# Performance work log

Measured on AMD Instinct MI355X. Metric: run time of the kernel, lower is better.

Reference implementation:

```python
import jax, jax.numpy as jnp
import numpy as np

N, E, B = 50000, 400000, 128
F_IN, EDIM, EMB, H = 64, 8, 64, 4
HC = EMB * H  # 256
L = 3          # gnn_layers
DN = 256       # dense_neurons
NEG_SLOPE = 0.2
EPS = 1e-5


def setup_inputs():
    key = jax.random.key(0)
    ks = jax.random.split(key, 32)
    s = 0.05
    d = {}
    d["x"] = jax.random.normal(ks[0], (N, F_IN), jnp.float32)
    d["edge_index"] = jax.random.randint(ks[1], (2, E), 0, N, jnp.int32)
    d["edge_attr"] = jax.random.normal(ks[2], (E, EDIM), jnp.float32)
    d["mol_formal_charge"] = jax.random.normal(ks[3], (B,), jnp.float32)
    d["mol_nrot"] = jax.random.normal(ks[4], (B,), jnp.float32)
    d["batch_index"] = jnp.sort(jax.random.randint(ks[5], (N,), 0, B, jnp.int32))
    # GATv2 params, stacked over L layers (in_dim == EMB == F_IN for all layers)
    d["gat_Wl"] = jax.random.normal(ks[6], (L, F_IN, HC), jnp.float32) * s
    d["gat_Wr"] = jax.random.normal(ks[7], (L, F_IN, HC), jnp.float32) * s
    d["gat_We"] = jax.random.normal(ks[8], (L, EDIM, HC), jnp.float32) * s
    d["gat_att"] = jax.random.normal(ks[9], (L, H, EMB), jnp.float32) * s
    d["gat_b"] = jnp.zeros((L, HC), jnp.float32)
    d["tr_W"] = jax.random.normal(ks[10], (L, HC, EMB), jnp.float32) * s
    d["tr_b"] = jnp.zeros((L, EMB), jnp.float32)
    d["bn_g"] = jnp.ones((L, EMB), jnp.float32)
    d["bn_b"] = jnp.zeros((L, EMB), jnp.float32)
    d["gate_W"] = jax.random.normal(ks[11], (EMB, 1), jnp.float32) * s
    d["gate_b"] = jnp.zeros((1,), jnp.float32)
    d["lin1_W"] = jax.random.normal(ks[12], (EMB + 2, DN), jnp.float32) * s
    d["lin1_b"] = jnp.zeros((DN,), jnp.float32)
    d["fc1_W"] = jax.random.normal(ks[13], (DN, DN // 2), jnp.float32) * s
    d["fc1_b"] = jnp.zeros((DN // 2,), jnp.float32)
    d["fc2_W"] = jax.random.normal(ks[14], (DN // 2, DN // 4), jnp.float32) * s
    d["fc2_b"] = jnp.zeros((DN // 4,), jnp.float32)
    d["out_W"] = jax.random.normal(ks[15], (DN // 4, 1), jnp.float32) * s
    d["out_b"] = jnp.zeros((1,), jnp.float32)
    return d


def _seg_softmax(logits, seg, num):
    # numerically stable per-segment softmax over leading axis
    mx = jax.ops.segment_max(logits, seg, num_segments=num)
    ex = jnp.exp(logits - mx[seg])
    den = jax.ops.segment_sum(ex, seg, num_segments=num)
    return ex / den[seg]


def reference(x, edge_index, edge_attr, mol_formal_charge, mol_nrot, batch_index,
              gat_Wl, gat_Wr, gat_We, gat_att, gat_b, tr_W, tr_b, bn_g, bn_b,
              gate_W, gate_b, lin1_W, lin1_b, fc1_W, fc1_b, fc2_W, fc2_b,
              out_W, out_b):
    src, dst = edge_index[0], edge_index[1]  # messages flow src -> dst
    h = x
    for l in range(L):
        xl = (h @ gat_Wl[l]).reshape(N, H, EMB)
        xr = (h @ gat_Wr[l]).reshape(N, H, EMB)
        ea = (edge_attr @ gat_We[l]).reshape(E, H, EMB)
        xls = xl[src]                                   # [E,H,C]
        m = jax.nn.leaky_relu(xls + xr[dst] + ea, NEG_SLOPE)
        logit = jnp.einsum('ehc,hc->eh', m, gat_att[l])  # [E,H]
        alpha = _seg_softmax(logit, dst, N)              # [E,H]
        agg = jax.ops.segment_sum(alpha[:, :, None] * xls, dst, num_segments=N)
        h = agg.reshape(N, HC) + gat_b[l]
        h = jax.nn.relu(h @ tr_W[l] + tr_b[l])
        # BatchNorm1d (training-mode batch stats, biased var)
        mu = h.mean(0)
        var = h.var(0)
        h = (h - mu) / jnp.sqrt(var + EPS) * bn_g[l] + bn_b[l]
    # AttentionalAggregation pooling
    gate = h @ gate_W + gate_b                           # [N,1]
    w = _seg_softmax(gate, batch_index, B)
    pooled = jax.ops.segment_sum(w * h, batch_index, num_segments=B)  # [B,EMB]
    z = jnp.concatenate([pooled, mol_formal_charge[:, None], mol_nrot[:, None]], axis=1)
    z = jax.nn.relu(z @ lin1_W + lin1_b)
    z = jax.nn.relu(z @ fc1_W + fc1_b)
    z = jax.nn.relu(z @ fc2_W + fc2_b)
    return z @ out_W + out_b                             # [B,1]
```

## Files before the change

### kernel.cpp

```cpp
#include <hip/hip_runtime.h>

#define NN 50000
#define NE 400000
#define NB 128
#define NINF (-__builtin_inff())

__device__ __forceinline__ float dpp_add16(float x) {
    int v = __float_as_int(x);
    x += __int_as_float(__builtin_amdgcn_update_dpp(0, v, 0xB1, 0xF, 0xF, true));
    v = __float_as_int(x);
    x += __int_as_float(__builtin_amdgcn_update_dpp(0, v, 0x4E, 0xF, 0xF, true));
    v = __float_as_int(x);
    x += __int_as_float(__builtin_amdgcn_update_dpp(0, v, 0x141, 0xF, 0xF, true));
    v = __float_as_int(x);
    x += __int_as_float(__builtin_amdgcn_update_dpp(0, v, 0x140, 0xF, 0xF, true));
    return x;
}

__global__ __launch_bounds__(256) void k_hist(const int* __restrict__ dstv, int* __restrict__ deg) {
    int e = blockIdx.x * 256 + threadIdx.x;
    if (e < NE) atomicAdd(&deg[dstv[e]], 1);
}

__global__ __launch_bounds__(256) void k_scan1(const int* __restrict__ deg, int* __restrict__ bsum) {
    __shared__ int ws[4];
    const int tid = threadIdx.x, lane = tid & 63, w = tid >> 6;
    const int i = blockIdx.x * 256 + tid;
    int v = (i < NN) ? deg[i] : 0;
    #pragma unroll
    for (int off = 32; off; off >>= 1) v += __shfl_xor(v, off);
    if (lane == 0) ws[w] = v;
    __syncthreads();
    if (tid == 0) bsum[blockIdx.x] = ws[0] + ws[1] + ws[2] + ws[3];
}

__global__ __launch_bounds__(256) void k_scan2(const int* __restrict__ bsum, int* __restrict__ boff, int nblk) {
    __shared__ int ws[4];
    const int tid = threadIdx.x, lane = tid & 63, w = tid >> 6;
    int v = (tid < nblk) ? bsum[tid] : 0;
    int incl = v;
    #pragma unroll
    for (int off = 1; off < 64; off <<= 1) {
        int t = __shfl_up(incl, off);
        if (lane >= off) incl += t;
    }
    if (lane == 63) ws[w] = incl;
    __syncthreads();
    int add = 0;
    for (int k = 0; k < w; ++k) add += ws[k];
    if (tid < nblk) boff[tid] = add + incl - v;
}

__global__ __launch_bounds__(256) void k_scan3(const int* __restrict__ deg, const int* __restrict__ boff,
                                               int* __restrict__ rowptr) {
    __shared__ int ws[4];
    const int tid = threadIdx.x, lane = tid & 63, w = tid >> 6;
    const int i = blockIdx.x * 256 + tid;
    int v = (i < NN) ? deg[i] : 0;
    int incl = v;
    #pragma unroll
    for (int off = 1; off < 64; off <<= 1) {
        int t = __shfl_up(incl, off);
        if (lane >= off) incl += t;
    }
    if (lane == 63) ws[w] = incl;
    __syncthreads();
    int add = boff[blockIdx.x];
    for (int k = 0; k < w; ++k) add += ws[k];
    if (i < NN) rowptr[i + 1] = add + incl;
    if (i == 0) rowptr[0] = 0;
}

__global__ __launch_bounds__(256) void k_scatter(const int* __restrict__ dstv, const int* __restrict__ srcv,
                                                 const float* __restrict__ eattr, const int* __restrict__ rowptr,
                                                 int* __restrict__ cnt, int* __restrict__ eid,
                                                 int* __restrict__ src_perm, float4* __restrict__ ea_perm,
                                                 int use_perm) {
    int e = blockIdx.x * 256 + threadIdx.x;
    if (e < NE) {
        int d = dstv[e];
        int pos = rowptr[d] + atomicAdd(&cnt[d], 1);
        eid[pos] = e;
        if (use_perm) {
            src_perm[pos] = srcv[e];
            ea_perm[(size_t)pos * 2] = ((const float4*)eattr)[e * 2];
            ea_perm[(size_t)pos * 2 + 1] = ((const float4*)eattr)[e * 2 + 1];
        }
    }
}

__global__ __launch_bounds__(256, 4) void k_gemm64(const float* __restrict__ A, const float* __restrict__ Wl,
                                                   const float* __restrict__ Wr, float* __restrict__ Cl,
                                                   float* __restrict__ Cr, const float* __restrict__ stats,
                                                   const float* __restrict__ bg, const float* __restrict__ bb) {
    __shared__ float At[32 * 132];
    __shared__ float Ws[32 * 128];
    __shared__ float sc_s[64], sh_s[64], shW_s[128];
    const int tid = threadIdx.x;
    const int mat = blockIdx.y >> 1, ch = blockIdx.y & 1;
    const float* W = mat ? Wr : Wl;
    float* C = mat ? Cr : Cl;
    const int r0b = blockIdx.x * 128;
    const int cg = tid & 15;
    const int rg = tid >> 4;

    if (stats) {
        if (tid < 64) {
            const float mu = stats[tid] * (1.0f / (float)NN);
            const float var = stats[64 + tid] * (1.0f / (float)NN) - mu * mu;
            const float rstd = rsqrtf(var + 1e-5f);
            const float sc = bg[tid] * rstd;
            sc_s[tid] = sc;
            sh_s[tid] = fmaf(-mu, sc, bb[tid]);
        }
        __syncthreads();
        if (tid < 128) {
            const float* wc = W + ch * 128 + tid;
            float s = 0.f;
            for (int k = 0; k < 64; ++k) s = fmaf(sh_s[k], wc[k * 256], s);
            shW_s[tid] = s;
        }
        __syncthreads();
    }

    float acc[8][8];
    if (stats) {
        #pragma unroll
        for (int rr = 0; rr < 8; ++rr)
            #pragma unroll
            for (int j = 0; j < 8; ++j)
                acc[rr][j] = (j < 4) ? shW_s[cg * 4 + j] : shW_s[64 + cg * 4 + (j - 4)];
    } else {
        #pragma unroll
        for (int rr = 0; rr < 8; ++rr)
            #pragma unroll
            for (int j = 0; j < 8; ++j) acc[rr][j] = 0.f;
    }

    for (int kc = 0; kc < 2; ++kc) {
        if (kc) __syncthreads();
        for (int i = tid; i < 1024; i += 256) {
            const int k = i >> 5, c4 = i & 31;
            float4 v = ((const float4*)W)[(kc * 32 + k) * 64 + ch * 32 + c4];
            if (stats) {
                const float s = sc_s[kc * 32 + k];
                v.x *= s; v.y *= s; v.z *= s; v.w *= s;
            }
            ((float4*)Ws)[i] = v;
        }
        for (int i = tid; i < 1024; i += 256) {
            const int r = i >> 3, c4 = i & 7;
            const int rgl = (r0b + r < NN) ? (r0b + r) : (NN - 1);
            const float4 v = ((const float4*)A)[rgl * 16 + kc * 8 + c4];
            At[(c4 * 4 + 0) * 132 + r] = v.x;
            At[(c4 * 4 + 1) * 132 + r] = v.y;
            At[(c4 * 4 + 2) * 132 + r] = v.z;
            At[(c4 * 4 + 3) * 132 + r] = v.w;
        }
        __syncthreads();
        #pragma unroll 4
        for (int k = 0; k < 32; ++k) {
            const float4 a0 = *(const float4*)(At + k * 132 + rg * 8);
            const float4 a1 = *(const float4*)(At + k * 132 + rg * 8 + 4);
            const float4 w0 = *(const float4*)(Ws + k * 128 + cg * 4);
            const float4 w1 = *(const float4*)(Ws + k * 128 + 64 + cg * 4);
            const float ar[8] = {a0.x, a0.y, a0.z, a0.w, a1.x, a1.y, a1.z, a1.w};
            #pragma unroll
            for (int rr = 0; rr < 8; ++rr) {
                acc[rr][0] = fmaf(ar[rr], w0.x, acc[rr][0]);
                acc[rr][1] = fmaf(ar[rr], w0.y, acc[rr][1]);
                acc[rr][2] = fmaf(ar[rr], w0.z, acc[rr][2]);
                acc[rr][3] = fmaf(ar[rr], w0.w, acc[rr][3]);
                acc[rr][4] = fmaf(ar[rr], w1.x, acc[rr][4]);
                acc[rr][5] = fmaf(ar[rr], w1.y, acc[rr][5]);
                acc[rr][6] = fmaf(ar[rr], w1.z, acc[rr][6]);
                acc[rr][7] = fmaf(ar[rr], w1.w, acc[rr][7]);
            }
        }
    }
    #pragma unroll
    for (int rr = 0; rr < 8; ++rr) {
        const int r = r0b + rg * 8 + rr;
        if (r < NN) {
            float* cp = C + (size_t)r * 256 + ch * 128 + cg * 4;
            *(float4*)cp = make_float4(acc[rr][0], acc[rr][1], acc[rr][2], acc[rr][3]);
            *(float4*)(cp + 64) = make_float4(acc[rr][4], acc[rr][5], acc[rr][6], acc[rr][7]);
        }
    }
}

template <bool PERM>
__global__ __launch_bounds__(256, 4) void k_agg(const float* __restrict__ xl, float* __restrict__ xragg,
                                                const float* __restrict__ att, const float* __restrict__ gatb,
                                                const int* __restrict__ rowptr, const int* __restrict__ eid,
                                                const int* __restrict__ srcv, const float* __restrict__ eattr,
                                                const int* __restrict__ src_perm, const float4* __restrict__ ea_perm,
                                                const float* __restrict__ We) {
    const int lane = threadIdx.x & 63;
    const float4 we0 = ((const float4*)(We + 0 * 256))[lane];
    const float4 we1 = ((const float4*)(We + 1 * 256))[lane];
    const float4 we2 = ((const float4*)(We + 2 * 256))[lane];
    const float4 we3 = ((const float4*)(We + 3 * 256))[lane];
    const float4 we4 = ((const float4*)(We + 4 * 256))[lane];
    const float4 we5 = ((const float4*)(We + 5 * 256))[lane];
    const float4 we6 = ((const float4*)(We + 6 * 256))[lane];
    const float4 we7 = ((const float4*)(We + 7 * 256))[lane];
    const float4 attf = ((const float4*)att)[lane];
    const float4 gbf = ((const float4*)gatb)[lane];
    const int nw = gridDim.x * (blockDim.x >> 6);
    int wid = blockIdx.x * (blockDim.x >> 6) + (threadIdx.x >> 6);

#define LOADE(X, idx)                                                          \
    {                                                                          \
        int s_;                                                                \
        const float4* eap_;                                                    \
        if (PERM) {                                                            \
            s_ = src_perm[idx];                                                \
            eap_ = ea_perm + (size_t)(idx) * 2;                                \
        } else {                                                               \
            const int e_ = eid[idx];                                           \
            s_ = srcv[e_];                                                     \
            eap_ = (const float4*)(eattr + (size_t)e_ * 8);                    \
        }                                                                      \
        X##x = ((const float4*)(xl + (size_t)s_ * 256))[lane];                 \
        X##a = eap_[0];                                                        \
        X##b = eap_[1];                                                        \
    }

#define PROC(X)                                                                \
    {                                                                          \
        float v0 = fmaf(X##a.x, we0.x, xr.x), v1 = fmaf(X##a.x, we0.y, xr.y);  \
        float v2 = fmaf(X##a.x, we0.z, xr.z), v3 = fmaf(X##a.x, we0.w, xr.w);  \
        v0 = fmaf(X##a.y, we1.x, v0); v1 = fmaf(X##a.y, we1.y, v1);            \
        v2 = fmaf(X##a.y, we1.z, v2); v3 = fmaf(X##a.y, we1.w, v3);            \
        v0 = fmaf(X##a.z, we2.x, v0); v1 = fmaf(X##a.z, we2.y, v1);            \
        v2 = fmaf(X##a.z, we2.z, v2); v3 = fmaf(X##a.z, we2.w, v3);            \
        v0 = fmaf(X##a.w, we3.x, v0); v1 = fmaf(X##a.w, we3.y, v1);            \
        v2 = fmaf(X##a.w, we3.z, v2); v3 = fmaf(X##a.w, we3.w, v3);            \
        v0 = fmaf(X##b.x, we4.x, v0); v1 = fmaf(X##b.x, we4.y, v1);            \
        v2 = fmaf(X##b.x, we4.z, v2); v3 = fmaf(X##b.x, we4.w, v3);            \
        v0 = fmaf(X##b.y, we5.x, v0); v1 = fmaf(X##b.y, we5.y, v1);            \
        v2 = fmaf(X##b.y, we5.z, v2); v3 = fmaf(X##b.y, we5.w, v3);            \
        v0 = fmaf(X##b.z, we6.x, v0); v1 = fmaf(X##b.z, we6.y, v1);            \
        v2 = fmaf(X##b.z, we6.z, v2); v3 = fmaf(X##b.z, we6.w, v3);            \
        v0 = fmaf(X##b.w, we7.x, v0); v1 = fmaf(X##b.w, we7.y, v1);            \
        v2 = fmaf(X##b.w, we7.z, v2); v3 = fmaf(X##b.w, we7.w, v3);            \
        v0 += X##x.x; v1 += X##x.y; v2 += X##x.z; v3 += X##x.w;                \
        v0 = fmaxf(v0, 0.2f * v0); v1 = fmaxf(v1, 0.2f * v1);                  \
        v2 = fmaxf(v2, 0.2f * v2); v3 = fmaxf(v3, 0.2f * v3);                  \
        float part = v0 * attf.x;                                              \
        part = fmaf(v1, attf.y, part);                                         \
        part = fmaf(v2, attf.z, part);                                         \
        part = fmaf(v3, attf.w, part);                                         \
        part = dpp_add16(part);                                                \
        const float p = __expf(part);                                          \
        den += p;                                                              \
        c0 = fmaf(p, X##x.x, c0);                                              \
        c1 = fmaf(p, X##x.y, c1);                                              \
        c2 = fmaf(p, X##x.z, c2);                                              \
        c3 = fmaf(p, X##x.w, c3);                                              \
    }

    for (int n = wid; n < NN; n += nw) {
        const int e0 = rowptr[n], e1 = rowptr[n + 1];
        const float4 xr = ((const float4*)(xragg + (size_t)n * 256))[lane];
        float den = 0.f, c0 = 0.f, c1 = 0.f, c2 = 0.f, c3 = 0.f;
        float4 Ax, Aa, Ab, Bx, Ba, Bb, Cx, Ca, Cb;
        const int cnt = e1 - e0;
        if (cnt > 0) {
            LOADE(A, e0);
            if (cnt > 1) LOADE(B, e0 + 1);
            if (cnt > 2) LOADE(C, e0 + 2);
            int i = e0;
            for (; i + 5 < e1; i += 3) {
                PROC(A);
                LOADE(A, i + 3);
                PROC(B);
                LOADE(B, i + 4);
                PROC(C);
                LOADE(C, i + 5);
            }
            const int m = e1 - i;
            PROC(A);
            if (m >= 2) PROC(B);
            if (m >= 3) PROC(C);
            if (m >= 4) { LOADE(A, i + 3); PROC(A); }
            if (m == 5) { LOADE(B, i + 4); PROC(B); }
        }
        float4 o;
        if (cnt > 0) {
            const float inv = 1.0f / den;
            o.x = fmaf(c0, inv, gbf.x);
            o.y = fmaf(c1, inv, gbf.y);
            o.z = fmaf(c2, inv, gbf.z);
            o.w = fmaf(c3, inv, gbf.w);
        } else {
            o = gbf;
        }
        ((float4*)(xragg + (size_t)n * 256))[lane] = o;
    }
#undef LOADE
#undef PROC
}

__global__ __launch_bounds__(256, 4) void k_tr(const float* __restrict__ A, const float* __restrict__ W,
                                               const float* __restrict__ bias, float* __restrict__ Hout,
                                               float* __restrict__ stats) {
    __shared__ float At[32 * 260];
    __shared__ float Ws[32 * 64];
    __shared__ float red[128];
    const int tid = threadIdx.x;
    const int cg = tid & 7;
    const int rg = tid >> 3;
    const int r0b = blockIdx.x * 256;

    float acc[8][8];
    #pragma unroll
    for (int rr = 0; rr < 8; ++rr)
        #pragma unroll
        for (int j = 0; j < 8; ++j)
            acc[rr][j] = bias[cg * 8 + j];

    for (int kc = 0; kc < 8; ++kc) {
        if (kc) __syncthreads();
        for (int i = tid; i < 512; i += 256)
            ((float4*)Ws)[i] = ((const float4*)(W + kc * 2048))[i];
        for (int i = tid; i < 2048; i += 256) {
            const int r = i >> 3, c4 = i & 7;
            const int rgl = (r0b + r < NN) ? (r0b + r) : (NN - 1);
            const float4 v = ((const float4*)A)[(size_t)rgl * 64 + kc * 8 + c4];
            At[(c4 * 4 + 0) * 260 + r] = v.x;
            At[(c4 * 4 + 1) * 260 + r] = v.y;
            At[(c4 * 4 + 2) * 260 + r] = v.z;
            At[(c4 * 4 + 3) * 260 + r] = v.w;
        }
        __syncthreads();
        #pragma unroll 4
        for (int k = 0; k < 32; ++k) {
            const float4 a0 = *(const float4*)(At + k * 260 + rg * 8);
            const float4 a1 = *(const float4*)(At + k * 260 + rg * 8 + 4);
            const float4 w0 = *(const float4*)(Ws + k * 64 + cg * 8);
            const float4 w1 = *(const float4*)(Ws + k * 64 + cg * 8 + 4);
            const float ar[8] = {a0.x, a0.y, a0.z, a0.w, a1.x, a1.y, a1.z, a1.w};
            #pragma unroll
            for (int rr = 0; rr < 8; ++rr) {
                acc[rr][0] = fmaf(ar[rr], w0.x, acc[rr][0]);
                acc[rr][1] = fmaf(ar[rr], w0.y, acc[rr][1]);
                acc[rr][2] = fmaf(ar[rr], w0.z, acc[rr][2]);
                acc[rr][3] = fmaf(ar[rr], w0.w, acc[rr][3]);
                acc[rr][4] = fmaf(ar[rr], w1.x, acc[rr][4]);
                acc[rr][5] = fmaf(ar[rr], w1.y, acc[rr][5]);
                acc[rr][6] = fmaf(ar[rr], w1.z, acc[rr][6]);
                acc[rr][7] = fmaf(ar[rr], w1.w, acc[rr][7]);
            }
        }
    }
    float lsum[8], lsq[8];
    #pragma unroll
    for (int j = 0; j < 8; ++j) { lsum[j] = 0.f; lsq[j] = 0.f; }
    #pragma unroll
    for (int rr = 0; rr < 8; ++rr) {
        const int r = r0b + rg * 8 + rr;
        if (r < NN) {
            float v[8];
            #pragma unroll
            for (int j = 0; j < 8; ++j) {
                v[j] = fmaxf(acc[rr][j], 0.f);
                lsum[j] += v[j];
                lsq[j] = fmaf(v[j], v[j], lsq[j]);
            }
            float* hp = Hout + (size_t)r * 64;
            *(float4*)(hp + cg * 8) = make_float4(v[0], v[1], v[2], v[3]);
            *(float4*)(hp + cg * 8 + 4) = make_float4(v[4], v[5], v[6], v[7]);
        }
    }
    __syncthreads();
    if (tid < 128) red[tid] = 0.f;
    __syncthreads();
    #pragma unroll
    for (int j = 0; j < 8; ++j) {
        atomicAdd(&red[cg * 8 + j], lsum[j]);
        atomicAdd(&red[64 + cg * 8 + j], lsq[j]);
    }
    __syncthreads();
    if (tid < 64) {
        atomicAdd(&stats[tid], red[tid]);
        atomicAdd(&stats[64 + tid], red[64 + tid]);
    }
}

__global__ __launch_bounds__(256) void k_poolhead(const float* __restrict__ h, const float* __restrict__ gw,
                                                  const int* __restrict__ bidx, const float* __restrict__ stats,
                                                  const float* __restrict__ bg, const float* __restrict__ bb,
                                                  const float* __restrict__ fc, const float* __restrict__ nrot,
                                                  const float* __restrict__ W1, const float* __restrict__ b1,
                                                  const float* __restrict__ W2, const float* __restrict__ b2,
                                                  const float* __restrict__ W3, const float* __restrict__ b3,
                                                  const float* __restrict__ W4, const float* __restrict__ b4,
                                                  float* __restrict__ out) {
    __shared__ float gate_s[1024];
    __shared__ float red[4];
    __shared__ float pp[4][64];
    __shared__ float scb[64], shb[64];
    __shared__ float z[66], a1[256], a2[128], a3[64];
    const int b = blockIdx.x, tid = threadIdx.x, lane = tid & 63, w = tid >> 6;
    if (tid < 64) {
        const float mu = stats[tid] * (1.0f / (float)NN);
        const float var = stats[64 + tid] * (1.0f / (float)NN) - mu * mu;
        const float rstd = rsqrtf(var + 1e-5f);
        const float sc = bg[tid] * rstd;
        scb[tid] = sc;
        shb[tid] = fmaf(-mu, sc, bb[tid]);
    }
    int lo = 0, hi = NN;
    while (lo < hi) { int mid = (lo + hi) >> 1; if (bidx[mid] < b) lo = mid + 1; else hi = mid; }
    const int s0 = lo;
    lo = 0; hi = NN;
    while (lo < hi) { int mid = (lo + hi) >> 1; if (bidx[mid] < b + 1) lo = mid + 1; else hi = mid; }
    const int s1 = lo;
    const int seg = s1 - s0;
    __syncthreads();

    const float gwv = gw[lane] * scb[lane];
    for (int i = s0 + w; i < s1; i += 4) {
        float p = h[(size_t)i * 64 + lane] * gwv;
        #pragma unroll
        for (int off = 32; off; off >>= 1) p += __shfl_xor(p, off);
        if (lane == 0) gate_s[i - s0] = p;
    }
    __syncthreads();
    float v = NINF;
    for (int i = tid; i < seg; i += 256) v = fmaxf(v, gate_s[i]);
    #pragma unroll
    for (int off = 32; off; off >>= 1) v = fmaxf(v, __shfl_xor(v, off));
    if (lane == 0) red[w] = v;
    __syncthreads();
    const float mx = fmaxf(fmaxf(red[0], red[1]), fmaxf(red[2], red[3]));
    __syncthreads();
    float d = 0.f;
    for (int i = tid; i < seg; i += 256) {
        const float ex = __expf(gate_s[i] - mx);
        gate_s[i] = ex;
        d += ex;
    }
    #pragma unroll
    for (int off = 32; off; off >>= 1) d += __shfl_xor(d, off);
    if (lane == 0) red[w] = d;
    __syncthreads();
    const float den = red[0] + red[1] + red[2] + red[3];
    const int c = tid & 63, ro = tid >> 6;
    float acc = 0.f;
    for (int i = s0 + ro; i < s1; i += 4) acc = fmaf(gate_s[i - s0], h[(size_t)i * 64 + c], acc);
    pp[ro][c] = acc;
    __syncthreads();
    if (tid < 64) {
        const float raw = (pp[0][tid] + pp[1][tid] + pp[2][tid] + pp[3][tid]) / den;
        z[tid] = (seg > 0) ? fmaf(raw, scb[tid], shb[tid]) : shb[tid];
    }
    if (tid == 64) z[64] = fc[b];
    if (tid == 65) z[65] = nrot[b];
    __syncthreads();
    float s = b1[tid];
    for (int k = 0; k < 66; ++k) s = fmaf(z[k], W1[k * 256 + tid], s);
    a1[tid] = fmaxf(s, 0.f);
    __syncthreads();
    if (tid < 128) {
        float s2 = b2[tid];
        for (int k = 0; k < 256; ++k) s2 = fmaf(a1[k], W2[k * 128 + tid], s2);
        a2[tid] = fmaxf(s2, 0.f);
    }
    __syncthreads();
    if (tid < 64) {
        float s3 = b3[tid];
        for (int k = 0; k < 128; ++k) s3 = fmaf(a2[k], W3[k * 64 + tid], s3);
        a3[tid] = fmaxf(s3, 0.f);
    }
    __syncthreads();
    if (tid < 64) {
        float p = a3[tid] * W4[tid];
        #pragma unroll
        for (int off = 32; off; off >>= 1) p += __shfl_xor(p, off);
        if (tid == 0) out[b] = p + b4[0];
    }
}

extern "C" void kernel_launch(void* const* d_in, const int* in_sizes, int n_in,
                              void* d_out, int out_size, void* d_ws, size_t ws_size,
                              hipStream_t stream) {
    const float* x     = (const float*)d_in[0];
    const int*   ei    = (const int*)d_in[1];
    const float* eattr = (const float*)d_in[2];
    const float* fcv   = (const float*)d_in[3];
    const float* nrot  = (const float*)d_in[4];
    const int*   bidx  = (const int*)d_in[5];
    const float* Wl    = (const float*)d_in[6];
    const float* Wr    = (const float*)d_in[7];
    const float* We    = (const float*)d_in[8];
    const float* att   = (const float*)d_in[9];
    const float* gatb  = (const float*)d_in[10];
    const float* trW   = (const float*)d_in[11];
    const float* trb   = (const float*)d_in[12];
    const float* bng   = (const float*)d_in[13];
    const float* bnb   = (const float*)d_in[14];
    const float* gateW = (const float*)d_in[15];
    const float* W1    = (const float*)d_in[17];
    const float* b1    = (const float*)d_in[18];
    const float* W2    = (const float*)d_in[19];
    const float* b2    = (const float*)d_in[20];
    const float* W3    = (const float*)d_in[21];
    const float* b3    = (const float*)d_in[22];
    const float* W4    = (const float*)d_in[23];
    const float* b4    = (const float*)d_in[24];
    float* out = (float*)d_out;

    const int* srcv = ei;
    const int* dstv = ei + NE;

    char* w = (char*)d_ws;
    float*  xl       = (float*)(w);
    float*  xragg    = (float*)(w + 51200000);
    float*  hbuf     = (float*)(w + 102400000);
    int*    deg      = (int*)  (w + 102400000);
    int*    cnt      = (int*)  (w + 102600000);
    int*    eid      = (int*)  (w + 115200000);
    int*    rowptr   = (int*)  (w + 116800000);
    float*  stats    = (float*)(w + 117000064);
    int*    bsum     = (int*)  (w + 117004096);
    int*    boff     = (int*)  (w + 117006144);
    int*    src_perm = (int*)  (w + 117042048);
    float4* ea_perm  = (float4*)(w + 118642048);
    const bool use_perm = (ws_size >= (size_t)131442048);
    const int NBLK = (NN + 255) / 256;

    hipMemsetAsync(deg, 0, 400000, stream);
    hipMemsetAsync(stats, 0, 1536, stream);
    k_hist<<<(NE + 255) / 256, 256, 0, stream>>>(dstv, deg);
    k_scan1<<<NBLK, 256, 0, stream>>>(deg, bsum);
    k_scan2<<<1, 256, 0, stream>>>(bsum, boff, NBLK);
    k_scan3<<<NBLK, 256, 0, stream>>>(deg, boff, rowptr);
    k_scatter<<<(NE + 255) / 256, 256, 0, stream>>>(dstv, srcv, eattr, rowptr, cnt, eid,
                                                    src_perm, ea_perm, use_perm ? 1 : 0);

    const float* hin = x;
    for (int l = 0; l < 3; ++l) {
        const float* st = (l == 0) ? nullptr : (stats + (l - 1) * 128);
        const float* g  = (l == 0) ? nullptr : (bng + (l - 1) * 64);
        const float* bb = (l == 0) ? nullptr : (bnb + (l - 1) * 64);
        dim3 gg((NN + 127) / 128, 4);
        k_gemm64<<<gg, 256, 0, stream>>>(hin, Wl + l * 16384, Wr + l * 16384, xl, xragg, st, g, bb);
        if (use_perm)
            k_agg<true><<<2048, 256, 0, stream>>>(xl, xragg, att + l * 256, gatb + l * 256, rowptr,
                                                  eid, srcv, eattr, src_perm, ea_perm, We + l * 2048);
        else
            k_agg<false><<<2048, 256, 0, stream>>>(xl, xragg, att + l * 256, gatb + l * 256, rowptr,
                                                   eid, srcv, eattr, src_perm, ea_perm, We + l * 2048);
        k_tr<<<(NN + 255) / 256, 256, 0, stream>>>(xragg, trW + l * 16384, trb + l * 64, hbuf, stats + l * 128);
        hin = hbuf;
    }
    k_poolhead<<<NB, 256, 0, stream>>>(hbuf, gateW, bidx, stats + 2 * 128, bng + 128, bnb + 128,
                                       fcv, nrot, W1, b1, W2, b2, W3, b3, W4, b4, out);
}
```

Before: 698.6 us.

## Prefetch next node's metadata in GAT aggregation and fold memsets into scan kernels

New measurement: 713.2 us. 2.1% more time.

```diff
diff --git a/kernel.cpp b/kernel.cpp
--- a/kernel.cpp
+++ b/kernel.cpp
@@ -22,10 +22,12 @@
     if (e < NE) atomicAdd(&deg[dstv[e]], 1);
 }
 
-__global__ __launch_bounds__(256) void k_scan1(const int* __restrict__ deg, int* __restrict__ bsum) {
+__global__ __launch_bounds__(256) void k_scan1(const int* __restrict__ deg, int* __restrict__ bsum,
+                                               int* __restrict__ cnt) {
     __shared__ int ws[4];
     const int tid = threadIdx.x, lane = tid & 63, w = tid >> 6;
     const int i = blockIdx.x * 256 + tid;
+    if (i < NN) cnt[i] = 0;
     int v = (i < NN) ? deg[i] : 0;
     #pragma unroll
     for (int off = 32; off; off >>= 1) v += __shfl_xor(v, off);
@@ -34,9 +36,11 @@
     if (tid == 0) bsum[blockIdx.x] = ws[0] + ws[1] + ws[2] + ws[3];
 }
 
-__global__ __launch_bounds__(256) void k_scan2(const int* __restrict__ bsum, int* __restrict__ boff, int nblk) {
+__global__ __launch_bounds__(256) void k_scan2(const int* __restrict__ bsum, int* __restrict__ boff, int nblk,
+                                               float* __restrict__ stats) {
     __shared__ int ws[4];
     const int tid = threadIdx.x, lane = tid & 63, w = tid >> 6;
+    for (int i = tid; i < 384; i += 256) stats[i] = 0.f;
     int v = (tid < nblk) ? bsum[tid] : 0;
     int incl = v;
     #pragma unroll
@@ -208,7 +212,7 @@
     const float4 attf = ((const float4*)att)[lane];
     const float4 gbf = ((const float4*)gatb)[lane];
     const int nw = gridDim.x * (blockDim.x >> 6);
-    int wid = blockIdx.x * (blockDim.x >> 6) + (threadIdx.x >> 6);
+    const int wid = blockIdx.x * (blockDim.x >> 6) + (threadIdx.x >> 6);
 
 #define LOADE(X, idx)                                                          \
     {                                                                          \
@@ -261,9 +265,19 @@
         c3 = fmaf(p, X##x.w, c3);                                              \
     }
 
-    for (int n = wid; n < NN; n += nw) {
-        const int e0 = rowptr[n], e1 = rowptr[n + 1];
-        const float4 xr = ((const float4*)(xragg + (size_t)n * 256))[lane];
+    int n = wid;
+    if (n >= NN) return;
+    float4 xr = ((const float4*)(xragg + (size_t)n * 256))[lane];
+    int e0 = rowptr[n], e1 = rowptr[n + 1];
+    while (true) {
+        const int n2 = n + nw;
+        float4 xr2;
+        int e02 = 0, e12 = 0;
+        if (n2 < NN) {
+            xr2 = ((const float4*)(xragg + (size_t)n2 * 256))[lane];
+            e02 = rowptr[n2];
+            e12 = rowptr[n2 + 1];
+        }
         float den = 0.f, c0 = 0.f, c1 = 0.f, c2 = 0.f, c3 = 0.f;
         float4 Ax, Aa, Ab, Bx, Ba, Bb, Cx, Ca, Cb;
         const int cnt = e1 - e0;
@@ -298,6 +312,8 @@
             o = gbf;
         }
         ((float4*)(xragg + (size_t)n * 256))[lane] = o;
+        if (n2 >= NN) break;
+        n = n2; xr = xr2; e0 = e02; e1 = e12;
     }
 #undef LOADE
 #undef PROC
@@ -532,11 +548,10 @@
     const bool use_perm = (ws_size >= (size_t)131442048);
     const int NBLK = (NN + 255) / 256;
 
-    hipMemsetAsync(deg, 0, 400000, stream);
-    hipMemsetAsync(stats, 0, 1536, stream);
+    hipMemsetAsync(deg, 0, 200000, stream);
     k_hist<<<(NE + 255) / 256, 256, 0, stream>>>(dstv, deg);
-    k_scan1<<<NBLK, 256, 0, stream>>>(deg, bsum);
-    k_scan2<<<1, 256, 0, stream>>>(bsum, boff, NBLK);
+    k_scan1<<<NBLK, 256, 0, stream>>>(deg, bsum, cnt);
+    k_scan2<<<1, 256, 0, stream>>>(bsum, boff, NBLK, stats);
     k_scan3<<<NBLK, 256, 0, stream>>>(deg, boff, rowptr);
     k_scatter<<<(NE + 255) / 256, 256, 0, stream>>>(dstv, srcv, eattr, rowptr, cnt, eid,
                                                     src_perm, ea_perm, use_perm ? 1 : 0);
@@ -549,10 +564,10 @@
         dim3 gg((NN + 127) / 128, 4);
         k_gemm64<<<gg, 256, 0, stream>>>(hin, Wl + l * 16384, Wr + l * 16384, xl, xragg, st, g, bb);
         if (use_perm)
-            k_agg<true><<<2048, 256, 0, stream>>>(xl, xragg, att + l * 256, gatb + l * 256, rowptr,
+            k_agg<true><<<4096, 256, 0, stream>>>(xl, xragg, att + l * 256, gatb + l * 256, rowptr,
                                                   eid, srcv, eattr, src_perm, ea_perm, We + l * 2048);
         else
-            k_agg<false><<<2048, 256, 0, stream>>>(xl, xragg, att + l * 256, gatb + l * 256, rowptr,
+            k_agg<false><<<4096, 256, 0, stream>>>(xl, xragg, att + l * 256, gatb + l * 256, rowptr,
                                                    eid, srcv, eattr, src_perm, ea_perm, We + l * 2048);
         k_tr<<<(NN + 255) / 256, 256, 0, stream>>>(xragg, trW + l * 16384, trb + l * 64, hbuf, stats + l * 128);
         hin = hbuf;
```

## Hoist BatchNorm fold into tiny kernel, shrink GEMM K-tiles, fold memsets into scans

Applied to the files above, without the earlier changes.

New measurement: 1.394 ms. +99.5%, slower.

```diff
diff --git a/kernel.cpp b/kernel.cpp
--- a/kernel.cpp
+++ b/kernel.cpp
@@ -22,10 +22,12 @@
     if (e < NE) atomicAdd(&deg[dstv[e]], 1);
 }
 
-__global__ __launch_bounds__(256) void k_scan1(const int* __restrict__ deg, int* __restrict__ bsum) {
+__global__ __launch_bounds__(256) void k_scan1(const int* __restrict__ deg, int* __restrict__ bsum,
+                                               int* __restrict__ cnt) {
     __shared__ int ws[4];
     const int tid = threadIdx.x, lane = tid & 63, w = tid >> 6;
     const int i = blockIdx.x * 256 + tid;
+    if (i < NN) cnt[i] = 0;
     int v = (i < NN) ? deg[i] : 0;
     #pragma unroll
     for (int off = 32; off; off >>= 1) v += __shfl_xor(v, off);
@@ -34,9 +36,11 @@
     if (tid == 0) bsum[blockIdx.x] = ws[0] + ws[1] + ws[2] + ws[3];
 }
 
-__global__ __launch_bounds__(256) void k_scan2(const int* __restrict__ bsum, int* __restrict__ boff, int nblk) {
+__global__ __launch_bounds__(256) void k_scan2(const int* __restrict__ bsum, int* __restrict__ boff, int nblk,
+                                               float* __restrict__ stats) {
     __shared__ int ws[4];
     const int tid = threadIdx.x, lane = tid & 63, w = tid >> 6;
+    for (int i = tid; i < 2304; i += 256) stats[i] = 0.f;
     int v = (tid < nblk) ? bsum[tid] : 0;
     int incl = v;
     #pragma unroll
@@ -89,13 +93,36 @@
     }
 }
 
-__global__ __launch_bounds__(256, 4) void k_gemm64(const float* __restrict__ A, const float* __restrict__ Wl,
+__global__ __launch_bounds__(256) void k_bnfin(float* __restrict__ st, const float* __restrict__ g,
+                                               const float* __restrict__ b, const float* __restrict__ Wln,
+                                               const float* __restrict__ Wrn) {
+    __shared__ float sh_s[64];
+    const int tid = threadIdx.x;
+    if (tid < 64) {
+        const float mu = st[tid] * (1.0f / (float)NN);
+        const float var = st[64 + tid] * (1.0f / (float)NN) - mu * mu;
+        const float rstd = rsqrtf(var + 1e-5f);
+        const float sc = g[tid] * rstd;
+        const float sh = fmaf(-mu, sc, b[tid]);
+        st[128 + tid] = sc;
+        st[192 + tid] = sh;
+        sh_s[tid] = sh;
+    }
+    __syncthreads();
+    float al = 0.f, ar = 0.f;
+    for (int k = 0; k < 64; ++k) {
+        al = fmaf(sh_s[k], Wln[k * 256 + tid], al);
+        ar = fmaf(sh_s[k], Wrn[k * 256 + tid], ar);
+    }
+    st[256 + tid] = al;
+    st[512 + tid] = ar;
+}
+
+__global__ __launch_bounds__(256, 5) void k_gemm64(const float* __restrict__ A, const float* __restrict__ Wl,
                                                    const float* __restrict__ Wr, float* __restrict__ Cl,
-                                                   float* __restrict__ Cr, const float* __restrict__ stats,
-                                                   const float* __restrict__ bg, const float* __restrict__ bb) {
-    __shared__ float At[32 * 132];
-    __shared__ float Ws[32 * 128];
-    __shared__ float sc_s[64], sh_s[64], shW_s[128];
+                                                   float* __restrict__ Cr, const float* __restrict__ stats) {
+    __shared__ float At[16 * 132];
+    __shared__ float Ws[16 * 128];
     const int tid = threadIdx.x;
     const int mat = blockIdx.y >> 1, ch = blockIdx.y & 1;
     const float* W = mat ? Wr : Wl;
@@ -104,32 +131,16 @@
     const int cg = tid & 15;
     const int rg = tid >> 4;
 
-    if (stats) {
-        if (tid < 64) {
-            const float mu = stats[tid] * (1.0f / (float)NN);
-            const float var = stats[64 + tid] * (1.0f / (float)NN) - mu * mu;
-            const float rstd = rsqrtf(var + 1e-5f);
-            const float sc = bg[tid] * rstd;
-            sc_s[tid] = sc;
-            sh_s[tid] = fmaf(-mu, sc, bb[tid]);
-        }
-        __syncthreads();
-        if (tid < 128) {
-            const float* wc = W + ch * 128 + tid;
-            float s = 0.f;
-            for (int k = 0; k < 64; ++k) s = fmaf(sh_s[k], wc[k * 256], s);
-            shW_s[tid] = s;
-        }
-        __syncthreads();
-    }
-
     float acc[8][8];
     if (stats) {
+        const float* shW = stats + 256 + mat * 256 + ch * 128;
+        const float4 i0 = *(const float4*)(shW + cg * 4);
+        const float4 i1 = *(const float4*)(shW + 64 + cg * 4);
         #pragma unroll
-        for (int rr = 0; rr < 8; ++rr)
-            #pragma unroll
-            for (int j = 0; j < 8; ++j)
-                acc[rr][j] = (j < 4) ? shW_s[cg * 4 + j] : shW_s[64 + cg * 4 + (j - 4)];
+        for (int rr = 0; rr < 8; ++rr) {
+            acc[rr][0] = i0.x; acc[rr][1] = i0.y; acc[rr][2] = i0.z; acc[rr][3] = i0.w;
+            acc[rr][4] = i1.x; acc[rr][5] = i1.y; acc[rr][6] = i1.z; acc[rr][7] = i1.w;
+        }
     } else {
         #pragma unroll
         for (int rr = 0; rr < 8; ++rr)
@@ -137,21 +148,21 @@
             for (int j = 0; j < 8; ++j) acc[rr][j] = 0.f;
     }
 
-    for (int kc = 0; kc < 2; ++kc) {
+    for (int kc = 0; kc < 4; ++kc) {
         if (kc) __syncthreads();
-        for (int i = tid; i < 1024; i += 256) {
+        for (int i = tid; i < 512; i += 256) {
             const int k = i >> 5, c4 = i & 31;
-            float4 v = ((const float4*)W)[(kc * 32 + k) * 64 + ch * 32 + c4];
+            float4 v = ((const float4*)W)[(kc * 16 + k) * 64 + ch * 32 + c4];
             if (stats) {
-                const float s = sc_s[kc * 32 + k];
+                const float s = stats[128 + kc * 16 + k];
                 v.x *= s; v.y *= s; v.z *= s; v.w *= s;
             }
             ((float4*)Ws)[i] = v;
         }
-        for (int i = tid; i < 1024; i += 256) {
-            const int r = i >> 3, c4 = i & 7;
+        for (int i = tid; i < 512; i += 256) {
+            const int r = i >> 2, c4 = i & 3;
             const int rgl = (r0b + r < NN) ? (r0b + r) : (NN - 1);
-            const float4 v = ((const float4*)A)[rgl * 16 + kc * 8 + c4];
+            const float4 v = ((const float4*)A)[rgl * 16 + kc * 4 + c4];
             At[(c4 * 4 + 0) * 132 + r] = v.x;
             At[(c4 * 4 + 1) * 132 + r] = v.y;
             At[(c4 * 4 + 2) * 132 + r] = v.z;
@@ -159,7 +170,7 @@
         }
         __syncthreads();
         #pragma unroll 4
-        for (int k = 0; k < 32; ++k) {
+        for (int k = 0; k < 16; ++k) {
             const float4 a0 = *(const float4*)(At + k * 132 + rg * 8);
             const float4 a1 = *(const float4*)(At + k * 132 + rg * 8 + 4);
             const float4 w0 = *(const float4*)(Ws + k * 128 + cg * 4);
@@ -208,7 +219,7 @@
     const float4 attf = ((const float4*)att)[lane];
     const float4 gbf = ((const float4*)gatb)[lane];
     const int nw = gridDim.x * (blockDim.x >> 6);
-    int wid = blockIdx.x * (blockDim.x >> 6) + (threadIdx.x >> 6);
+    const int wid = blockIdx.x * (blockDim.x >> 6) + (threadIdx.x >> 6);
 
 #define LOADE(X, idx)                                                          \
     {                                                                          \
@@ -303,11 +314,11 @@
 #undef PROC
 }
 
-__global__ __launch_bounds__(256, 4) void k_tr(const float* __restrict__ A, const float* __restrict__ W,
+__global__ __launch_bounds__(256, 5) void k_tr(const float* __restrict__ A, const float* __restrict__ W,
                                                const float* __restrict__ bias, float* __restrict__ Hout,
                                                float* __restrict__ stats) {
-    __shared__ float At[32 * 260];
-    __shared__ float Ws[32 * 64];
+    __shared__ float At[16 * 260];
+    __shared__ float Ws[16 * 64];
     __shared__ float red[128];
     const int tid = threadIdx.x;
     const int cg = tid & 7;
@@ -321,14 +332,13 @@
         for (int j = 0; j < 8; ++j)
             acc[rr][j] = bias[cg * 8 + j];
 
-    for (int kc = 0; kc < 8; ++kc) {
+    for (int kc = 0; kc < 16; ++kc) {
         if (kc) __syncthreads();
-        for (int i = tid; i < 512; i += 256)
-            ((float4*)Ws)[i] = ((const float4*)(W + kc * 2048))[i];
-        for (int i = tid; i < 2048; i += 256) {
-            const int r = i >> 3, c4 = i & 7;
+        if (tid < 256) ((float4*)Ws)[tid] = ((const float4*)(W + kc * 1024))[tid];
+        for (int i = tid; i < 1024; i += 256) {
+            const int r = i >> 2, c4 = i & 3;
             const int rgl = (r0b + r < NN) ? (r0b + r) : (NN - 1);
-            const float4 v = ((const float4*)A)[(size_t)rgl * 64 + kc * 8 + c4];
+            const float4 v = ((const float4*)A)[(size_t)rgl * 64 + kc * 4 + c4];
             At[(c4 * 4 + 0) * 260 + r] = v.x;
             At[(c4 * 4 + 1) * 260 + r] = v.y;
             At[(c4 * 4 + 2) * 260 + r] = v.z;
@@ -336,7 +346,7 @@
         }
         __syncthreads();
         #pragma unroll 4
-        for (int k = 0; k < 32; ++k) {
+        for (int k = 0; k < 16; ++k) {
             const float4 a0 = *(const float4*)(At + k * 260 + rg * 8);
             const float4 a1 = *(const float4*)(At + k * 260 + rg * 8 + 4);
             const float4 w0 = *(const float4*)(Ws + k * 64 + cg * 8);
@@ -525,38 +535,38 @@
     int*    eid      = (int*)  (w + 115200000);
     int*    rowptr   = (int*)  (w + 116800000);
     float*  stats    = (float*)(w + 117000064);
-    int*    bsum     = (int*)  (w + 117004096);
-    int*    boff     = (int*)  (w + 117006144);
+    int*    bsum     = (int*)  (w + 117010176);
+    int*    boff     = (int*)  (w + 117012224);
     int*    src_perm = (int*)  (w + 117042048);
     float4* ea_perm  = (float4*)(w + 118642048);
     const bool use_perm = (ws_size >= (size_t)131442048);
     const int NBLK = (NN + 255) / 256;
 
-    hipMemsetAsync(deg, 0, 400000, stream);
-    hipMemsetAsync(stats, 0, 1536, stream);
+    hipMemsetAsync(deg, 0, 200000, stream);
     k_hist<<<(NE + 255) / 256, 256, 0, stream>>>(dstv, deg);
-    k_scan1<<<NBLK, 256, 0, stream>>>(deg, bsum);
-    k_scan2<<<1, 256, 0, stream>>>(bsum, boff, NBLK);
+    k_scan1<<<NBLK, 256, 0, stream>>>(deg, bsum, cnt);
+    k_scan2<<<1, 256, 0, stream>>>(bsum, boff, NBLK, stats);
     k_scan3<<<NBLK, 256, 0, stream>>>(deg, boff, rowptr);
     k_scatter<<<(NE + 255) / 256, 256, 0, stream>>>(dstv, srcv, eattr, rowptr, cnt, eid,
                                                     src_perm, ea_perm, use_perm ? 1 : 0);
 
     const float* hin = x;
     for (int l = 0; l < 3; ++l) {
-        const float* st = (l == 0) ? nullptr : (stats + (l - 1) * 128);
-        const float* g  = (l == 0) ? nullptr : (bng + (l - 1) * 64);
-        const float* bb = (l == 0) ? nullptr : (bnb + (l - 1) * 64);
+        const float* st = (l == 0) ? nullptr : (stats + (l - 1) * 768);
         dim3 gg((NN + 127) / 128, 4);
-        k_gemm64<<<gg, 256, 0, stream>>>(hin, Wl + l * 16384, Wr + l * 16384, xl, xragg, st, g, bb);
+        k_gemm64<<<gg, 256, 0, stream>>>(hin, Wl + l * 16384, Wr + l * 16384, xl, xragg, st);
         if (use_perm)
             k_agg<true><<<2048, 256, 0, stream>>>(xl, xragg, att + l * 256, gatb + l * 256, rowptr,
                                                   eid, srcv, eattr, src_perm, ea_perm, We + l * 2048);
         else
             k_agg<false><<<2048, 256, 0, stream>>>(xl, xragg, att + l * 256, gatb + l * 256, rowptr,
                                                    eid, srcv, eattr, src_perm, ea_perm, We + l * 2048);
-        k_tr<<<(NN + 255) / 256, 256, 0, stream>>>(xragg, trW + l * 16384, trb + l * 64, hbuf, stats + l * 128);
+        k_tr<<<(NN + 255) / 256, 256, 0, stream>>>(xragg, trW + l * 16384, trb + l * 64, hbuf, stats + l * 768);
+        if (l < 2)
+            k_bnfin<<<1, 256, 0, stream>>>(stats + l * 768, bng + l * 64, bnb + l * 64,
+                                           Wl + (l + 1) * 16384, Wr + (l + 1) * 16384);
         hin = hbuf;
     }
-    k_poolhead<<<NB, 256, 0, stream>>>(hbuf, gateW, bidx, stats + 2 * 128, bng + 128, bnb + 128,
+    k_poolhead<<<NB, 256, 0, stream>>>(hbuf, gateW, bidx, stats + 2 * 768, bng + 128, bnb + 128,
                                        fcv, nrot, W1, b1, W2, b2, W3, b3, W4, b4, out);
 }
```
